# Kernel tuning notes

Hardware: AMD Instinct MI355X
Metric: run time of the kernel (lower is better)

Reference implementation:

```python
import jax, jax.numpy as jnp
import numpy as np

D_K = 64
SCALE = 1.0 / (D_K ** 0.5)
NEG_INF = float('-inf')


def setup_inputs() -> dict:
    key = jax.random.key(0)
    kq, kk, kv = jax.random.split(key, 3)
    B, H, S, D = 2, 16, 2048, D_K
    Q = jax.random.normal(kq, (B, H, S, D), dtype=jnp.float32)
    K = jax.random.normal(kk, (B, H, S, D), dtype=jnp.float32)
    V = jax.random.normal(kv, (B, H, S, D), dtype=jnp.float32)
    # causal mask: True = attend, False = masked (matches masked_fill(mask == False, -inf))
    mask = jnp.tril(jnp.ones((S, S), dtype=jnp.bool_))
    return {"Q": Q, "K": K, "V": V, "mask": mask}


def reference(Q, K, V, mask):
    # scores: [B, H, q, k]
    scores = jnp.einsum('bhqd,bhkd->bhqk', Q, K) * SCALE
    scores = jnp.where(mask, scores, NEG_INF)
    # hand-rolled stable softmax, same math as the torch module
    x_exp = jnp.exp(scores - jnp.max(scores, axis=-1, keepdims=True))
    attn = x_exp / jnp.sum(x_exp, axis=-1, keepdims=True)
    out = jnp.einsum('bhqk,bhkv->bhqv', attn, V)
    return out
```

## Files before the change

kernel.cpp:

```cpp
#include <hip/hip_runtime.h>
#include <hip/hip_bf16.h>

#define S_LEN   2048
#define D_DIM   64
#define BK      64
#define NBH     32

typedef __attribute__((ext_vector_type(8))) short  short8;
typedef __attribute__((ext_vector_type(4))) float  floatx4;

#define KLD   72
#define VTLD  72
#define PLD   72
#define OLD   65

#define VOFF  9216
#define POFF  18432
#define SMEM_BYTES 27648

__device__ __forceinline__ unsigned pk2(float lo, float hi) {
  __hip_bfloat162 h = __float22bfloat162_rn(float2{lo, hi});
  union { __hip_bfloat162 v; unsigned u; } c; c.v = h;
  return c.u;
}
__device__ __forceinline__ short8 pk8(const float* f) {
  union { short8 s; unsigned u[4]; } r;
  r.u[0] = pk2(f[0], f[1]); r.u[1] = pk2(f[2], f[3]);
  r.u[2] = pk2(f[4], f[5]); r.u[3] = pk2(f[6], f[7]);
  return r.s;
}
__device__ __forceinline__ float bf2f(unsigned short s) {
  union { unsigned u; float f; } c; c.u = ((unsigned)s) << 16; return c.f;
}

__global__ __launch_bounds__(256, 2)
void prep(const float* __restrict__ K, const float* __restrict__ V,
          unsigned short* __restrict__ Kbf, unsigned short* __restrict__ Vt)
{
  __shared__ unsigned short vt[64 * KLD];
  const int tid = threadIdx.x;
  const int bh  = blockIdx.x >> 5;
  const int k0  = (blockIdx.x & 31) * 64;

  {
    const int k   = k0 + (tid >> 2);
    const int seg = (tid & 3) * 16;
    const float* p = K + ((size_t)(bh * S_LEN + k)) * D_DIM + seg;
    union { float4 v[4]; float f[16]; } u;
    u.v[0] = *(const float4*)p;       u.v[1] = *(const float4*)(p + 4);
    u.v[2] = *(const float4*)(p + 8); u.v[3] = *(const float4*)(p + 12);
    unsigned short* dst = Kbf + ((size_t)(bh * S_LEN + k)) * D_DIM + seg;
    *(short8*)dst       = pk8(u.f);
    *(short8*)(dst + 8) = pk8(u.f + 8);
  }
  {
    const int kp2 = tid & 31;
    const int dg  = (tid >> 5) * 8;
    const float* p = V + ((size_t)(bh * S_LEN + k0 + 2 * kp2)) * D_DIM + dg;
    union { float4 v[2]; float f[8]; } x, y;
    x.v[0] = *(const float4*)p;            x.v[1] = *(const float4*)(p + 4);
    y.v[0] = *(const float4*)(p + D_DIM);  y.v[1] = *(const float4*)(p + D_DIM + 4);
#pragma unroll
    for (int i = 0; i < 8; ++i)
      *(unsigned*)&vt[(dg + i) * KLD + 2 * kp2] = pk2(x.f[i], y.f[i]);
  }
  __syncthreads();
  {
    const int d   = tid >> 2;
    const int seg = (tid & 3) * 16;
    short8 a = *(short8*)&vt[d * KLD + seg];
    short8 b = *(short8*)&vt[d * KLD + seg + 8];
    unsigned short* dst = Vt + ((size_t)(bh * D_DIM + d)) * S_LEN + k0 + seg;
    *(short8*)dst       = a;
    *(short8*)(dst + 8) = b;
  }
}

__global__ __launch_bounds__(256, 2)
void fa_fwd(const float* __restrict__ Qg,
            const unsigned short* __restrict__ Kbf,
            const unsigned short* __restrict__ Vt,
            float* __restrict__ Og,
            unsigned short* __restrict__ Opart,
            float* __restrict__ Lpart)
{
  __shared__ char smem[SMEM_BYTES];
  short* Klds  = (short*)smem;
  short* Vtlds = (short*)(smem + VOFF);

  const int tid  = threadIdx.x;
  const int wv   = tid >> 6;
  const int lane = tid & 63;
  const int col  = lane & 15;
  const int quad = lane >> 4;
  short* Plds = (short*)(smem + POFF) + wv * (16 * PLD);
  float* Olds = (float*)smem + wv * (16 * OLD);

  int qblk, bh, it0, itend, half = 0;
  bool split;
  if (blockIdx.x < 1024) {
    split = true;
    qblk  = 31 - ((int)blockIdx.x >> 6);
    bh    = ((int)blockIdx.x >> 1) & 31;
    half  = blockIdx.x & 1;
    const int nk = qblk + 1;
    const int h0 = (nk + 1) >> 1;
    it0   = half ? h0 : 0;
    itend = half ? nk : h0;
  } else {
    split = false;
    const int u = blockIdx.x - 1024;
    qblk  = 15 - (u >> 5);
    bh    = u & 31;
    it0   = 0;
    itend = qblk + 1;
  }

  const float qscale = 0.18033688011112042f;
  const float*          Qb  = Qg  + (size_t)bh * S_LEN * D_DIM;
  const unsigned short* Kb  = Kbf + (size_t)bh * S_LEN * D_DIM;
  const unsigned short* Vtb = Vt  + (size_t)bh * D_DIM * S_LEN;
  float*                Ob  = Og  + (size_t)bh * S_LEN * D_DIM;

  const int srow = tid >> 2;
  const int sseg = (tid & 3) * 16;

  const int q0 = qblk * 64;
  const int qw = q0 + wv * 16;

  short8 qf[2];
#pragma unroll
  for (int h = 0; h < 2; ++h) {
    const float* qp = Qb + (size_t)(qw + col) * D_DIM + h * 32 + quad * 8;
    union { float4 v[2]; float f[8]; } u;
    u.v[0] = *(const float4*)qp; u.v[1] = *(const float4*)(qp + 4);
    float t[8];
#pragma unroll
    for (int j = 0; j < 8; ++j) t[j] = u.f[j] * qscale;
    qf[h] = pk8(t);
  }

  floatx4 o[4];
#pragma unroll
  for (int dt = 0; dt < 4; ++dt) o[dt] = (floatx4){0.f,0.f,0.f,0.f};
  float l_run = 0.f;

  short8 kpre[2], vpre[2];
  {
    const unsigned short* kp = Kb  + (size_t)(it0 * BK + srow) * D_DIM + sseg;
    kpre[0] = *(const short8*)kp;  kpre[1] = *(const short8*)(kp + 8);
    const unsigned short* vp = Vtb + (size_t)srow * S_LEN + it0 * BK + sseg;
    vpre[0] = *(const short8*)vp;  vpre[1] = *(const short8*)(vp + 8);
  }

  for (int it = it0; it < itend; ++it) {
    __syncthreads();
    *(short8*)&Klds [srow * KLD  + sseg]     = kpre[0];
    *(short8*)&Klds [srow * KLD  + sseg + 8] = kpre[1];
    *(short8*)&Vtlds[srow * VTLD + sseg]     = vpre[0];
    *(short8*)&Vtlds[srow * VTLD + sseg + 8] = vpre[1];
    __syncthreads();

    if (it + 1 < itend) {
      const int kb2 = (it + 1) * BK;
      const unsigned short* kp = Kb  + (size_t)(kb2 + srow) * D_DIM + sseg;
      kpre[0] = *(const short8*)kp;  kpre[1] = *(const short8*)(kp + 8);
      const unsigned short* vp = Vtb + (size_t)srow * S_LEN + kb2 + sseg;
      vpre[0] = *(const short8*)vp;  vpre[1] = *(const short8*)(vp + 8);
    }

    short8 kf[4][2];
#pragma unroll
    for (int kt = 0; kt < 4; ++kt)
#pragma unroll
      for (int h = 0; h < 2; ++h)
        kf[kt][h] = *(short8*)&Klds[(kt * 16 + col) * KLD + h * 32 + quad * 8];

    floatx4 st[4];
#pragma unroll
    for (int kt = 0; kt < 4; ++kt) {
      floatx4 c = (floatx4){0.f,0.f,0.f,0.f};
      c = __builtin_amdgcn_mfma_f32_16x16x32_bf16(kf[kt][0], qf[0], c, 0, 0, 0);
      c = __builtin_amdgcn_mfma_f32_16x16x32_bf16(kf[kt][1], qf[1], c, 0, 0, 0);
      st[kt] = c;
    }

    if (it == qblk) {
      const int qg = qw + col;
      const int kb = it * BK;
#pragma unroll
      for (int kt = 0; kt < 4; ++kt)
#pragma unroll
        for (int r = 0; r < 4; ++r)
          if (kb + kt * 16 + quad * 4 + r > qg) st[kt][r] = -3.0e38f;
    }

    float lsum = 0.f;
#pragma unroll
    for (int kt = 0; kt < 4; ++kt)
#pragma unroll
      for (int r = 0; r < 4; ++r) {
        const float p = __builtin_amdgcn_exp2f(st[kt][r]);
        st[kt][r] = p;
        lsum += p;
      }
    l_run += lsum;

#pragma unroll
    for (int kt = 0; kt < 4; ++kt) {
      uint2 w; w.x = pk2(st[kt][0], st[kt][1]); w.y = pk2(st[kt][2], st[kt][3]);
      *(uint2*)&Plds[col * PLD + kt * 16 + quad * 4] = w;
    }
    short8 pf0 = *(short8*)&Plds[col * PLD + quad * 8];
    short8 pf1 = *(short8*)&Plds[col * PLD + 32 + quad * 8];

#pragma unroll
    for (int dt = 0; dt < 4; ++dt) {
      short8 vf0 = *(short8*)&Vtlds[(dt * 16 + col) * VTLD + quad * 8];
      short8 vf1 = *(short8*)&Vtlds[(dt * 16 + col) * VTLD + 32 + quad * 8];
      o[dt] = __builtin_amdgcn_mfma_f32_16x16x32_bf16(vf0, pf0, o[dt], 0, 0, 0);
      o[dt] = __builtin_amdgcn_mfma_f32_16x16x32_bf16(vf1, pf1, o[dt], 0, 0, 0);
    }
  }

  __syncthreads();
  float l = l_run;
  l += __shfl_xor(l, 16);
  l += __shfl_xor(l, 32);

  if (!split) {
    const float inv = 1.0f / l;
#pragma unroll
    for (int dt = 0; dt < 4; ++dt)
#pragma unroll
      for (int r = 0; r < 4; ++r)
        Olds[col * OLD + dt * 16 + quad * 4 + r] = o[dt][r] * inv;
#pragma unroll
    for (int it2 = 0; it2 < 4; ++it2) {
      const int ql = it2 * 4 + quad;
      float4 w;
      w.x = Olds[ql * OLD + col * 4 + 0];
      w.y = Olds[ql * OLD + col * 4 + 1];
      w.z = Olds[ql * OLD + col * 4 + 2];
      w.w = Olds[ql * OLD + col * 4 + 3];
      *(float4*)(Ob + (size_t)(qw + ql) * D_DIM + col * 4) = w;
    }
  } else {
#pragma unroll
    for (int dt = 0; dt < 4; ++dt)
#pragma unroll
      for (int r = 0; r < 4; ++r)
        Olds[col * OLD + dt * 16 + quad * 4 + r] = o[dt][r];
    const size_t pbase = (((size_t)(half * 32 + bh) * 16) + (qblk - 16)) * 4096;
#pragma unroll
    for (int it2 = 0; it2 < 4; ++it2) {
      const int ql = it2 * 4 + quad;
      float4 w;
      w.x = Olds[ql * OLD + col * 4 + 0];
      w.y = Olds[ql * OLD + col * 4 + 1];
      w.z = Olds[ql * OLD + col * 4 + 2];
      w.w = Olds[ql * OLD + col * 4 + 3];
      uint2 pw; pw.x = pk2(w.x, w.y); pw.y = pk2(w.z, w.w);
      *(uint2*)&Opart[pbase + (size_t)(wv * 16 + ql) * 64 + col * 4] = pw;
    }
    if (quad == 0)
      Lpart[(((half * 32 + bh) * 16) + (qblk - 16)) * 64 + wv * 16 + col] = l;
  }
}

__global__ __launch_bounds__(256, 2)
void merge(const unsigned short* __restrict__ Opart,
           const float* __restrict__ Lpart,
           float* __restrict__ Og)
{
  const int tid = threadIdx.x;
  const int gid = blockIdx.x * 64 + (tid >> 2);
  const int seg = (tid & 3) * 16;
  const int bh = gid >> 10;
  const int qs = (gid >> 6) & 15;
  const int ql = gid & 63;
  const float la = Lpart[((0 * 32 + bh) * 16 + qs) * 64 + ql];
  const float lb = Lpart[((1 * 32 + bh) * 16 + qs) * 64 + ql];
  const float inv = 1.0f / (la + lb);
  const unsigned short* pa = Opart + (((size_t)(0 * 32 + bh) * 16 + qs) * 4096 + ql * 64 + seg);
  const unsigned short* pb = Opart + (((size_t)(1 * 32 + bh) * 16 + qs) * 4096 + ql * 64 + seg);
  union { short8 s; unsigned short h[8]; } a0, a1, b0, b1;
  a0.s = *(short8*)pa; a1.s = *(short8*)(pa + 8);
  b0.s = *(short8*)pb; b1.s = *(short8*)(pb + 8);
  float out[16];
#pragma unroll
  for (int j = 0; j < 8; ++j) out[j]     = (bf2f(a0.h[j]) + bf2f(b0.h[j])) * inv;
#pragma unroll
  for (int j = 0; j < 8; ++j) out[8 + j] = (bf2f(a1.h[j]) + bf2f(b1.h[j])) * inv;
  float* dst = Og + ((size_t)bh * S_LEN + 1024 + qs * 64 + ql) * D_DIM + seg;
#pragma unroll
  for (int j = 0; j < 4; ++j)
    *(float4*)(dst + 4 * j) = *(float4*)&out[4 * j];
}

extern "C" void kernel_launch(void* const* d_in, const int* in_sizes, int n_in,
                              void* d_out, int out_size, void* d_ws, size_t ws_size,
                              hipStream_t stream) {
  const float* Q = (const float*)d_in[0];
  const float* K = (const float*)d_in[1];
  const float* V = (const float*)d_in[2];
  float* O = (float*)d_out;
  unsigned short* Kbf   = (unsigned short*)d_ws;
  unsigned short* Vt    = Kbf + (size_t)NBH * S_LEN * D_DIM;
  unsigned short* Opart = Vt  + (size_t)NBH * S_LEN * D_DIM;
  float*          Lpart = (float*)(Opart + (size_t)2 * 32 * 16 * 4096);

  hipLaunchKernelGGL(prep,   dim3(NBH * (S_LEN / 64)), dim3(256), 0, stream, K, V, Kbf, Vt);
  hipLaunchKernelGGL(fa_fwd, dim3(1536), dim3(256), 0, stream, Q, Kbf, Vt, O, Opart, Lpart);
  hipLaunchKernelGGL(merge,  dim3(512),  dim3(256), 0, stream, Opart, Lpart, O);
}
```

Measured before the change: 143.8 us.

## Process two 64-row query tiles per block to reuse K/V tiles

Each workgroup now handles 128 query rows, 64 per pair of wave tiles, instead of 64, so every K/V tile staged into LDS feeds twice as many MFMAs. The grid halves to 768 blocks, and the split/merge partial layout is re-indexed per query row. The first query tile's work is skipped on the diagonal block where it is fully masked. This cuts K/V global and LDS staging traffic per unit of work, but costs more registers, more LDS, fewer blocks and a coarser load balance.

```diff
diff --git a/kernel.cpp b/kernel.cpp
--- a/kernel.cpp
+++ b/kernel.cpp
@@ -16,7 +16,7 @@
 
 #define VOFF  9216
 #define POFF  18432
-#define SMEM_BYTES 27648
+#define SMEM_BYTES 36864
 
 __device__ __forceinline__ unsigned pk2(float lo, float hi) {
   __hip_bfloat162 h = __float22bfloat162_rn(float2{lo, hi});
@@ -93,28 +93,30 @@
   const int lane = tid & 63;
   const int col  = lane & 15;
   const int quad = lane >> 4;
-  short* Plds = (short*)(smem + POFF) + wv * (16 * PLD);
+  short* PA = (short*)(smem + POFF) + wv * (32 * PLD);
+  short* PB = PA + 16 * PLD;
   float* Olds = (float*)smem + wv * (16 * OLD);
 
-  int qblk, bh, it0, itend, half = 0;
+  int qi, bh, it0, itend, half = 0;
   bool split;
-  if (blockIdx.x < 1024) {
+  if (blockIdx.x < 512) {
     split = true;
-    qblk  = 31 - ((int)blockIdx.x >> 6);
+    qi    = 15 - ((int)blockIdx.x >> 6);
     bh    = ((int)blockIdx.x >> 1) & 31;
     half  = blockIdx.x & 1;
-    const int nk = qblk + 1;
-    const int h0 = (nk + 1) >> 1;
+    const int nk = 2 * (qi + 1);
+    const int h0 = nk >> 1;
     it0   = half ? h0 : 0;
     itend = half ? nk : h0;
   } else {
     split = false;
-    const int u = blockIdx.x - 1024;
-    qblk  = 15 - (u >> 5);
+    const int u = blockIdx.x - 512;
+    qi    = 7 - (u >> 5);
     bh    = u & 31;
     it0   = 0;
-    itend = qblk + 1;
-  }
+    itend = 2 * (qi + 1);
+  }
+  const int q0 = qi * 128;
 
   const float qscale = 0.18033688011112042f;
   const float*          Qb  = Qg  + (size_t)bh * S_LEN * D_DIM;
@@ -125,25 +127,28 @@
   const int srow = tid >> 2;
   const int sseg = (tid & 3) * 16;
 
-  const int q0 = qblk * 64;
-  const int qw = q0 + wv * 16;
-
-  short8 qf[2];
-#pragma unroll
-  for (int h = 0; h < 2; ++h) {
-    const float* qp = Qb + (size_t)(qw + col) * D_DIM + h * 32 + quad * 8;
-    union { float4 v[2]; float f[8]; } u;
-    u.v[0] = *(const float4*)qp; u.v[1] = *(const float4*)(qp + 4);
-    float t[8];
-#pragma unroll
-    for (int j = 0; j < 8; ++j) t[j] = u.f[j] * qscale;
-    qf[h] = pk8(t);
-  }
-
-  floatx4 o[4];
-#pragma unroll
-  for (int dt = 0; dt < 4; ++dt) o[dt] = (floatx4){0.f,0.f,0.f,0.f};
-  float l_run = 0.f;
+  const int qws[2] = {q0 + wv * 16, q0 + 64 + wv * 16};
+
+  short8 qf[2][2];
+#pragma unroll
+  for (int qt = 0; qt < 2; ++qt)
+#pragma unroll
+    for (int h = 0; h < 2; ++h) {
+      const float* qp = Qb + (size_t)(qws[qt] + col) * D_DIM + h * 32 + quad * 8;
+      union { float4 v[2]; float f[8]; } u;
+      u.v[0] = *(const float4*)qp; u.v[1] = *(const float4*)(qp + 4);
+      float t[8];
+#pragma unroll
+      for (int j = 0; j < 8; ++j) t[j] = u.f[j] * qscale;
+      qf[qt][h] = pk8(t);
+    }
+
+  floatx4 o[2][4];
+#pragma unroll
+  for (int qt = 0; qt < 2; ++qt)
+#pragma unroll
+    for (int dt = 0; dt < 4; ++dt) o[qt][dt] = (floatx4){0.f,0.f,0.f,0.f};
+  float l_run[2] = {0.f, 0.f};
 
   short8 kpre[2], vpre[2];
   {
@@ -169,102 +174,123 @@
       vpre[0] = *(const short8*)vp;  vpre[1] = *(const short8*)(vp + 8);
     }
 
-    short8 kf[4][2];
-#pragma unroll
-    for (int kt = 0; kt < 4; ++kt)
-#pragma unroll
-      for (int h = 0; h < 2; ++h)
-        kf[kt][h] = *(short8*)&Klds[(kt * 16 + col) * KLD + h * 32 + quad * 8];
-
-    floatx4 st[4];
+    const int  kb  = it * BK;
+    const bool doA = (kb != q0 + 64);
+
+    floatx4 st[2][4];
 #pragma unroll
     for (int kt = 0; kt < 4; ++kt) {
+      short8 kf0 = *(short8*)&Klds[(kt * 16 + col) * KLD + quad * 8];
+      short8 kf1 = *(short8*)&Klds[(kt * 16 + col) * KLD + 32 + quad * 8];
       floatx4 c = (floatx4){0.f,0.f,0.f,0.f};
-      c = __builtin_amdgcn_mfma_f32_16x16x32_bf16(kf[kt][0], qf[0], c, 0, 0, 0);
-      c = __builtin_amdgcn_mfma_f32_16x16x32_bf16(kf[kt][1], qf[1], c, 0, 0, 0);
-      st[kt] = c;
-    }
-
-    if (it == qblk) {
-      const int qg = qw + col;
-      const int kb = it * BK;
+      c = __builtin_amdgcn_mfma_f32_16x16x32_bf16(kf0, qf[1][0], c, 0, 0, 0);
+      c = __builtin_amdgcn_mfma_f32_16x16x32_bf16(kf1, qf[1][1], c, 0, 0, 0);
+      st[1][kt] = c;
+      if (doA) {
+        floatx4 d = (floatx4){0.f,0.f,0.f,0.f};
+        d = __builtin_amdgcn_mfma_f32_16x16x32_bf16(kf0, qf[0][0], d, 0, 0, 0);
+        d = __builtin_amdgcn_mfma_f32_16x16x32_bf16(kf1, qf[0][1], d, 0, 0, 0);
+        st[0][kt] = d;
+      }
+    }
+
+    if (kb == q0) {
+      const int qg = qws[0] + col;
 #pragma unroll
       for (int kt = 0; kt < 4; ++kt)
 #pragma unroll
         for (int r = 0; r < 4; ++r)
-          if (kb + kt * 16 + quad * 4 + r > qg) st[kt][r] = -3.0e38f;
-    }
-
-    float lsum = 0.f;
-#pragma unroll
-    for (int kt = 0; kt < 4; ++kt)
-#pragma unroll
-      for (int r = 0; r < 4; ++r) {
-        const float p = __builtin_amdgcn_exp2f(st[kt][r]);
-        st[kt][r] = p;
-        lsum += p;
-      }
-    l_run += lsum;
-
-#pragma unroll
-    for (int kt = 0; kt < 4; ++kt) {
-      uint2 w; w.x = pk2(st[kt][0], st[kt][1]); w.y = pk2(st[kt][2], st[kt][3]);
-      *(uint2*)&Plds[col * PLD + kt * 16 + quad * 4] = w;
-    }
-    short8 pf0 = *(short8*)&Plds[col * PLD + quad * 8];
-    short8 pf1 = *(short8*)&Plds[col * PLD + 32 + quad * 8];
-
-#pragma unroll
-    for (int dt = 0; dt < 4; ++dt) {
-      short8 vf0 = *(short8*)&Vtlds[(dt * 16 + col) * VTLD + quad * 8];
-      short8 vf1 = *(short8*)&Vtlds[(dt * 16 + col) * VTLD + 32 + quad * 8];
-      o[dt] = __builtin_amdgcn_mfma_f32_16x16x32_bf16(vf0, pf0, o[dt], 0, 0, 0);
-      o[dt] = __builtin_amdgcn_mfma_f32_16x16x32_bf16(vf1, pf1, o[dt], 0, 0, 0);
+          if (kb + kt * 16 + quad * 4 + r > qg) st[0][kt][r] = -3.0e38f;
+    }
+    if (!doA) {
+      const int qg = qws[1] + col;
+#pragma unroll
+      for (int kt = 0; kt < 4; ++kt)
+#pragma unroll
+        for (int r = 0; r < 4; ++r)
+          if (kb + kt * 16 + quad * 4 + r > qg) st[1][kt][r] = -3.0e38f;
+    }
+
+#pragma unroll
+    for (int qt = 0; qt < 2; ++qt) {
+      if (qt == 0 && !doA) continue;
+      float lsum = 0.f;
+#pragma unroll
+      for (int kt = 0; kt < 4; ++kt)
+#pragma unroll
+        for (int r = 0; r < 4; ++r) {
+          const float p = __builtin_amdgcn_exp2f(st[qt][kt][r]);
+          st[qt][kt][r] = p;
+          lsum += p;
+        }
+      l_run[qt] += lsum;
+      short* Pq = qt ? PB : PA;
+#pragma unroll
+      for (int kt = 0; kt < 4; ++kt) {
+        uint2 w; w.x = pk2(st[qt][kt][0], st[qt][kt][1]); w.y = pk2(st[qt][kt][2], st[qt][kt][3]);
+        *(uint2*)&Pq[col * PLD + kt * 16 + quad * 4] = w;
+      }
+    }
+
+#pragma unroll
+    for (int g = 0; g < 2; ++g) {
+      short8 pfB = *(short8*)&PB[col * PLD + g * 32 + quad * 8];
+      short8 pfA;
+      if (doA) pfA = *(short8*)&PA[col * PLD + g * 32 + quad * 8];
+#pragma unroll
+      for (int dt = 0; dt < 4; ++dt) {
+        short8 vf = *(short8*)&Vtlds[(dt * 16 + col) * VTLD + g * 32 + quad * 8];
+        o[1][dt] = __builtin_amdgcn_mfma_f32_16x16x32_bf16(vf, pfB, o[1][dt], 0, 0, 0);
+        if (doA)
+          o[0][dt] = __builtin_amdgcn_mfma_f32_16x16x32_bf16(vf, pfA, o[0][dt], 0, 0, 0);
+      }
     }
   }
 
   __syncthreads();
-  float l = l_run;
-  l += __shfl_xor(l, 16);
-  l += __shfl_xor(l, 32);
-
-  if (!split) {
-    const float inv = 1.0f / l;
-#pragma unroll
-    for (int dt = 0; dt < 4; ++dt)
-#pragma unroll
-      for (int r = 0; r < 4; ++r)
-        Olds[col * OLD + dt * 16 + quad * 4 + r] = o[dt][r] * inv;
-#pragma unroll
-    for (int it2 = 0; it2 < 4; ++it2) {
-      const int ql = it2 * 4 + quad;
-      float4 w;
-      w.x = Olds[ql * OLD + col * 4 + 0];
-      w.y = Olds[ql * OLD + col * 4 + 1];
-      w.z = Olds[ql * OLD + col * 4 + 2];
-      w.w = Olds[ql * OLD + col * 4 + 3];
-      *(float4*)(Ob + (size_t)(qw + ql) * D_DIM + col * 4) = w;
-    }
-  } else {
-#pragma unroll
-    for (int dt = 0; dt < 4; ++dt)
-#pragma unroll
-      for (int r = 0; r < 4; ++r)
-        Olds[col * OLD + dt * 16 + quad * 4 + r] = o[dt][r];
-    const size_t pbase = (((size_t)(half * 32 + bh) * 16) + (qblk - 16)) * 4096;
-#pragma unroll
-    for (int it2 = 0; it2 < 4; ++it2) {
-      const int ql = it2 * 4 + quad;
-      float4 w;
-      w.x = Olds[ql * OLD + col * 4 + 0];
-      w.y = Olds[ql * OLD + col * 4 + 1];
-      w.z = Olds[ql * OLD + col * 4 + 2];
-      w.w = Olds[ql * OLD + col * 4 + 3];
-      uint2 pw; pw.x = pk2(w.x, w.y); pw.y = pk2(w.z, w.w);
-      *(uint2*)&Opart[pbase + (size_t)(wv * 16 + ql) * 64 + col * 4] = pw;
-    }
-    if (quad == 0)
-      Lpart[(((half * 32 + bh) * 16) + (qblk - 16)) * 64 + wv * 16 + col] = l;
+#pragma unroll
+  for (int qt = 0; qt < 2; ++qt) {
+    float l = l_run[qt];
+    l += __shfl_xor(l, 16);
+    l += __shfl_xor(l, 32);
+    if (!split) {
+      const float inv = 1.0f / l;
+#pragma unroll
+      for (int dt = 0; dt < 4; ++dt)
+#pragma unroll
+        for (int r = 0; r < 4; ++r)
+          Olds[col * OLD + dt * 16 + quad * 4 + r] = o[qt][dt][r] * inv;
+#pragma unroll
+      for (int it2 = 0; it2 < 4; ++it2) {
+        const int ql = it2 * 4 + quad;
+        float4 w;
+        w.x = Olds[ql * OLD + col * 4 + 0];
+        w.y = Olds[ql * OLD + col * 4 + 1];
+        w.z = Olds[ql * OLD + col * 4 + 2];
+        w.w = Olds[ql * OLD + col * 4 + 3];
+        *(float4*)(Ob + (size_t)(qws[qt] + ql) * D_DIM + col * 4) = w;
+      }
+    } else {
+#pragma unroll
+      for (int dt = 0; dt < 4; ++dt)
+#pragma unroll
+        for (int r = 0; r < 4; ++r)
+          Olds[col * OLD + dt * 16 + quad * 4 + r] = o[qt][dt][r];
+#pragma unroll
+      for (int it2 = 0; it2 < 4; ++it2) {
+        const int ql = it2 * 4 + quad;
+        const int p  = qws[qt] + ql - 1024;
+        float4 w;
+        w.x = Olds[ql * OLD + col * 4 + 0];
+        w.y = Olds[ql * OLD + col * 4 + 1];
+        w.z = Olds[ql * OLD + col * 4 + 2];
+        w.w = Olds[ql * OLD + col * 4 + 3];
+        uint2 pw; pw.x = pk2(w.x, w.y); pw.y = pk2(w.z, w.w);
+        *(uint2*)&Opart[((size_t)(half * 32 + bh) * 1024 + p) * 64 + col * 4] = pw;
+      }
+      if (quad == 0)
+        Lpart[(half * 32 + bh) * 1024 + (qws[qt] + col - 1024)] = l;
+    }
   }
 }
 
@@ -276,14 +302,13 @@
   const int tid = threadIdx.x;
   const int gid = blockIdx.x * 64 + (tid >> 2);
   const int seg = (tid & 3) * 16;
-  const int bh = gid >> 10;
-  const int qs = (gid >> 6) & 15;
-  const int ql = gid & 63;
-  const float la = Lpart[((0 * 32 + bh) * 16 + qs) * 64 + ql];
-  const float lb = Lpart[((1 * 32 + bh) * 16 + qs) * 64 + ql];
+  const int bh  = gid >> 10;
+  const int p   = gid & 1023;
+  const float la = Lpart[(0 * 32 + bh) * 1024 + p];
+  const float lb = Lpart[(1 * 32 + bh) * 1024 + p];
   const float inv = 1.0f / (la + lb);
-  const unsigned short* pa = Opart + (((size_t)(0 * 32 + bh) * 16 + qs) * 4096 + ql * 64 + seg);
-  const unsigned short* pb = Opart + (((size_t)(1 * 32 + bh) * 16 + qs) * 4096 + ql * 64 + seg);
+  const unsigned short* pa = Opart + ((size_t)(0 * 32 + bh) * 1024 + p) * 64 + seg;
+  const unsigned short* pb = Opart + ((size_t)(1 * 32 + bh) * 1024 + p) * 64 + seg;
   union { short8 s; unsigned short h[8]; } a0, a1, b0, b1;
   a0.s = *(short8*)pa; a1.s = *(short8*)(pa + 8);
   b0.s = *(short8*)pb; b1.s = *(short8*)(pb + 8);
@@ -292,7 +317,7 @@
   for (int j = 0; j < 8; ++j) out[j]     = (bf2f(a0.h[j]) + bf2f(b0.h[j])) * inv;
 #pragma unroll
   for (int j = 0; j < 8; ++j) out[8 + j] = (bf2f(a1.h[j]) + bf2f(b1.h[j])) * inv;
-  float* dst = Og + ((size_t)bh * S_LEN + 1024 + qs * 64 + ql) * D_DIM + seg;
+  float* dst = Og + ((size_t)bh * S_LEN + 1024 + p) * D_DIM + seg;
 #pragma unroll
   for (int j = 0; j < 4; ++j)
     *(float4*)(dst + 4 * j) = *(float4*)&out[4 * j];
@@ -308,9 +333,9 @@
   unsigned short* Kbf   = (unsigned short*)d_ws;
   unsigned short* Vt    = Kbf + (size_t)NBH * S_LEN * D_DIM;
   unsigned short* Opart = Vt  + (size_t)NBH * S_LEN * D_DIM;
-  float*          Lpart = (float*)(Opart + (size_t)2 * 32 * 16 * 4096);
+  float*          Lpart = (float*)(Opart + (size_t)2 * 32 * 1024 * 64);
 
   hipLaunchKernelGGL(prep,   dim3(NBH * (S_LEN / 64)), dim3(256), 0, stream, K, V, Kbf, Vt);
-  hipLaunchKernelGGL(fa_fwd, dim3(1536), dim3(256), 0, stream, Q, Kbf, Vt, O, Opart, Lpart);
-  hipLaunchKernelGGL(merge,  dim3(512),  dim3(256), 0, stream, Opart, Lpart, O);
-}
+  hipLaunchKernelGGL(fa_fwd, dim3(768), dim3(256), 0, stream, Q, Kbf, Vt, O, Opart, Lpart);
+  hipLaunchKernelGGL(merge,  dim3(512), dim3(256), 0, stream, Opart, Lpart, O);
+}
```

Measured after the change: 141.4 us. No clear change (-1.6%).
